# Kernel tuning notes

Hardware: AMD Instinct MI355X
Metric: run time of the kernel (lower is better)

## Reference

```python
import jax, jax.numpy as jnp
import numpy as np

N_NODES = 50000
N_EDGES = 1600000
N_GRAPHS = 64
IN_DIM = 128
HID = 128
N_CLASSES = 10


def setup_inputs() -> dict:
    key = jax.random.key(0)
    ks = jax.random.split(key, 12)
    x = jax.random.normal(ks[0], (N_NODES, IN_DIM), dtype=jnp.float32)
    edge_index = jax.random.randint(ks[1], (2, N_EDGES), 0, N_NODES, dtype=jnp.int32)
    batch = jnp.sort(jax.random.randint(ks[2], (N_NODES,), 0, N_GRAPHS, dtype=jnp.int32))
    def glorot(k, shape):
        s = 1.0 / np.sqrt(shape[0])
        return jax.random.uniform(k, shape, jnp.float32, -s, s)
    W1 = glorot(ks[3], (IN_DIM, HID)); b1 = jnp.zeros((HID,), jnp.float32)
    W2 = glorot(ks[4], (HID, HID));    b2 = jnp.zeros((HID,), jnp.float32)
    Wc1 = glorot(ks[5], (HID, HID));   bc1 = glorot(ks[6], (HID,))
    Wc2 = glorot(ks[7], (HID, N_CLASSES)); bc2 = glorot(ks[8], (N_CLASSES,))
    return {"x": x, "edge_index": edge_index, "batch": batch,
            "W1": W1, "b1": b1, "W2": W2, "b2": b2,
            "Wc1": Wc1, "bc1": bc1, "Wc2": Wc2, "bc2": bc2}


def gcn_conv(x, edge_index, W, b):
    """PyG GCNConv: sym-normalized A-hat (with self loops) @ (x W) + b."""
    n = x.shape[0]
    loop = jnp.arange(n, dtype=edge_index.dtype)
    src = jnp.concatenate([edge_index[0], loop])  # message source
    dst = jnp.concatenate([edge_index[1], loop])  # message target
    deg = jax.ops.segment_sum(jnp.ones_like(src, dtype=x.dtype), dst, num_segments=n)
    dinv = jnp.where(deg > 0, jax.lax.rsqrt(deg), jnp.zeros_like(deg))
    norm = dinv[src] * dinv[dst]  # [E+N]
    h = x @ W                     # [N, H]
    msg = h[src] * norm[:, None]  # gather + scale
    out = jax.ops.segment_sum(msg, dst, num_segments=n)
    return out + b


def reference(x, edge_index, batch, W1, b1, W2, b2, Wc1, bc1, Wc2, bc2):
    h = jax.nn.relu(gcn_conv(x, edge_index, W1, b1))
    h = jax.nn.relu(gcn_conv(h, edge_index, W2, b2))
    # per-graph mean pooling (segment mean)
    sums = jax.ops.segment_sum(h, batch, num_segments=N_GRAPHS)
    cnt = jax.ops.segment_sum(jnp.ones((h.shape[0],), h.dtype), batch, num_segments=N_GRAPHS)
    g = sums / jnp.clip(cnt, 1.0)[:, None]  # [G, H]
    z = jax.nn.relu(g @ Wc1 + bc1)
    return z @ Wc2 + bc2
```

## Files before the change

kernel.cpp:

```cpp
#include <hip/hip_runtime.h>
#include <cstdint>
#include <cstddef>

#define CHUNK 8192

typedef __attribute__((ext_vector_type(8))) short short8;
typedef __attribute__((ext_vector_type(4))) float f32x4;
typedef __attribute__((ext_vector_type(2))) float f32x2;
typedef __attribute__((ext_vector_type(4))) unsigned int u32x4;

__device__ __forceinline__ float bf2f(unsigned short u) {
  return __uint_as_float(((unsigned)u) << 16);
}
__device__ __forceinline__ unsigned short f2bf(float f) {
  unsigned u = __float_as_uint(f);
  u += 0x7fffu + ((u >> 16) & 1u);
  return (unsigned short)(u >> 16);
}
__device__ __forceinline__ f32x2 unpk(unsigned u) {
  f32x2 r;
  r.x = __uint_as_float(u << 16);
  r.y = __uint_as_float(u & 0xffff0000u);
  return r;
}
__device__ __forceinline__ void pkfma(f32x2& a, f32x2 b, f32x2 c) {
  asm("v_pk_fma_f32 %0, %1, %2, %0" : "+v"(a) : "v"(b), "v"(c));
}

union SMem {
  unsigned short ws[128 * 136];
  struct { int c[256]; int cur[256]; int sb[256];
           unsigned short colL[12288]; } cf;
};

__global__ void prep_k(const float* __restrict__ W1, const float* __restrict__ W2,
                       unsigned short* __restrict__ W1t, unsigned short* __restrict__ W2t,
                       int* __restrict__ gcur, int B,
                       float* __restrict__ gsums, int GN) {
  int idx = blockIdx.x * 256 + threadIdx.x;
  const float* W = (idx < 16384) ? W1 : W2;
  unsigned short* Wt = (idx < 16384) ? W1t : W2t;
  int i = idx & 16383;
  int k = i >> 7, n = i & 127;
  Wt[n * 128 + k] = f2bf(W[i]);
  if (blockIdx.x == 0 && threadIdx.x < B) gcur[threadIdx.x] = 0;
  if (idx < GN) gsums[idx] = 0.f;
}

__global__ __launch_bounds__(512) void scatter_sort_k(const int* __restrict__ src,
                                                      const int* __restrict__ dst, int E,
                                                      int* __restrict__ gcur,
                                                      unsigned int* __restrict__ tmp,
                                                      int cap, int B) {
  __shared__ unsigned sorted[CHUNK];
  __shared__ int h[256];
  __shared__ int lps[256];
  __shared__ int base_s[256];
  __shared__ int cur[256];
  int t = threadIdx.x;
  if (t < 256) h[t] = 0;
  __syncthreads();
  int e0 = blockIdx.x * CHUNK;
  int e1 = e0 + CHUNK; if (e1 > E) e1 = E;
  int m = e1 - e0;
  for (int i = t; i < m; i += 512) {
    atomicAdd(&h[dst[e0 + i] >> 8], 1);
  }
  __syncthreads();
  int v = (t < 256) ? h[t] : 0;
  if (t < 256) lps[t] = v;
  __syncthreads();
  for (int off = 1; off < 256; off <<= 1) {
    int u = (t >= off && t < 256) ? lps[t - off] : 0;
    __syncthreads();
    if (t < 256) lps[t] += u;
    __syncthreads();
  }
  int incl = (t < 256) ? lps[t] : 0;
  if (t < B && v > 0) base_s[t] = atomicAdd(&gcur[t], v);
  if (t < 256) {
    cur[t] = 0;
    lps[t] = incl - v;
  }
  __syncthreads();
  for (int i = t; i < m; i += 512) {
    int d = dst[e0 + i], s = src[e0 + i];
    int b = d >> 8;
    int r = atomicAdd(&cur[b], 1);
    sorted[lps[b] + r] = ((unsigned)b << 24) | ((unsigned)s << 8) | (unsigned)(d & 255);
  }
  __syncthreads();
  for (int i = t; i < m; i += 512) {
    unsigned u = sorted[i];
    int b = u >> 24;
    int p = base_s[b] + (i - lps[b]);
    if (p < cap) tmp[(size_t)b * cap + p] = u;
  }
}

template <bool AF32>
__device__ __forceinline__ void gemm_tile(SMem& sm, const void* Ap,
                                          const unsigned short* Wt,
                                          unsigned short* C, int N, int tile) {
  for (int idx = threadIdx.x; idx < 2048; idx += 512) {
    int n = idx >> 4, c = idx & 15;
    *(uint4*)&sm.ws[n * 136 + c * 8] = ((const uint4*)Wt)[idx];
  }
  __syncthreads();
  const int w = threadIdx.x >> 6;
  const int lane = threadIdx.x & 63;
  const int quad = lane >> 4, l16 = lane & 15;
  const int r = tile * 128 + w * 16 + l16;
  f32x4 acc[8] = {};
  #pragma unroll
  for (int ks = 0; ks < 4; ks++) {
    short8 a = {};
    if (r < N) {
      if (AF32) {
        const float* ar = (const float*)Ap + (size_t)r * 128 + ks * 32 + quad * 8;
        float4 u0 = *(const float4*)ar;
        float4 u1 = *(const float4*)(ar + 4);
        a[0] = (short)f2bf(u0.x); a[1] = (short)f2bf(u0.y);
        a[2] = (short)f2bf(u0.z); a[3] = (short)f2bf(u0.w);
        a[4] = (short)f2bf(u1.x); a[5] = (short)f2bf(u1.y);
        a[6] = (short)f2bf(u1.z); a[7] = (short)f2bf(u1.w);
      } else {
        a = *(const short8*)((const unsigned short*)Ap + (size_t)r * 128 + ks * 32 + quad * 8);
      }
    }
    #pragma unroll
    for (int t = 0; t < 8; t++) {
      short8 bF = *(const short8*)&sm.ws[(t * 16 + l16) * 136 + ks * 32 + quad * 8];
      acc[t] = __builtin_amdgcn_mfma_f32_16x16x32_bf16(a, bF, acc[t], 0, 0, 0);
    }
  }
  __syncthreads();
  unsigned short* Cs = sm.ws;
  {
    int rloc = w * 16 + quad * 4;
    #pragma unroll
    for (int t = 0; t < 8; t++)
      #pragma unroll
      for (int rg = 0; rg < 4; rg++)
        Cs[(rloc + rg) * 132 + t * 16 + l16] = f2bf(acc[t][rg]);
  }
  __syncthreads();
  const int r0 = tile * 128;
  for (int idx = threadIdx.x; idx < 2048; idx += 512) {
    int row = idx >> 4, c = idx & 15;
    int rr = r0 + row;
    if (rr < N) {
      uint2 a = *(uint2*)&Cs[row * 132 + c * 8];
      uint2 b = *(uint2*)&Cs[row * 132 + c * 8 + 4];
      ((uint4*)C)[(size_t)rr * 16 + c] = make_uint4(a.x, a.y, b.x, b.y);
    }
  }
}

__global__ __launch_bounds__(512) void cntfill_gemm1_k(const unsigned int* __restrict__ tmp,
                                                       const int* __restrict__ gcur,
                                                       int N, int E, int cap, int B,
                                                       float* __restrict__ dinv,
                                                       int* __restrict__ rs,
                                                       unsigned short* __restrict__ col,
                                                       const float* __restrict__ x,
                                                       const unsigned short* __restrict__ W1t,
                                                       unsigned short* __restrict__ B2) {
  __shared__ SMem sm;
  const int t = threadIdx.x;
  if ((int)blockIdx.x >= B) {
    gemm_tile<true>(sm, x, W1t, B2, N, blockIdx.x - B);
    return;
  }
  int b = blockIdx.x;
  int cb = 0;
  if (t < B) { cb = gcur[t]; if (cb > cap) cb = cap; }
  if (t < 256) sm.cf.sb[t] = cb;
  __syncthreads();
  for (int off = 1; off < 256; off <<= 1) {
    int u = (t >= off && t < 256) ? sm.cf.sb[t - off] : 0;
    __syncthreads();
    if (t < 256) sm.cf.sb[t] += u;
    __syncthreads();
  }
  int base_b = (b > 0) ? sm.cf.sb[b - 1] : 0;
  int cnt_b = sm.cf.sb[b] - base_b;
  if (b == 0 && t == 0) rs[N] = sm.cf.sb[B - 1];
  const unsigned* tb = tmp + (size_t)b * cap;
  if (t < 256) sm.cf.c[t] = 0;
  __syncthreads();
  for (int i = t; i < cnt_b; i += 512) atomicAdd(&sm.cf.c[tb[i] & 255u], 1);
  __syncthreads();
  int v = (t < 256) ? sm.cf.c[t] : 0;
  if (t < 256) sm.cf.cur[t] = v;
  __syncthreads();
  for (int off = 1; off < 256; off <<= 1) {
    int u = (t >= off && t < 256) ? sm.cf.cur[t - off] : 0;
    __syncthreads();
    if (t < 256) sm.cf.cur[t] += u;
    __syncthreads();
  }
  int rsv = (t < 256) ? (base_b + sm.cf.cur[t] - v) : 0;
  int node = (b << 8) + t;
  if (t < 256 && node < N) {
    rs[node] = rsv;
    dinv[node] = rsqrtf((float)v + 1.0f);
  }
  __syncthreads();
  if (cnt_b <= 12288) {
    if (t < 256) sm.cf.cur[t] = rsv - base_b;
    __syncthreads();
    for (int i = t; i < cnt_b; i += 512) {
      unsigned u = tb[i];
      int lpos = atomicAdd(&sm.cf.cur[u & 255u], 1);
      sm.cf.colL[lpos] = (unsigned short)((u >> 8) & 0xFFFFu);
    }
    __syncthreads();
    for (int i = t; i < cnt_b; i += 512) col[base_b + i] = sm.cf.colL[i];
  } else {
    if (t < 256) sm.cf.cur[t] = rsv;
    __syncthreads();
    for (int i = t; i < cnt_b; i += 512) {
      unsigned u = tb[i];
      int pos = atomicAdd(&sm.cf.cur[u & 255u], 1);
      col[pos] = (unsigned short)((u >> 8) & 0xFFFFu);
    }
  }
}

template <bool AF32>
__global__ __launch_bounds__(512) void gemm_bf_k(const void* __restrict__ Ap,
                                                 const unsigned short* __restrict__ Wt,
                                                 unsigned short* __restrict__ C, int N) {
  __shared__ SMem sm;
  gemm_tile<AF32>(sm, Ap, Wt, C, N, blockIdx.x);
}

template <typename CT>
__device__ __forceinline__ void agg_body(f32x2 (&acc2)[4],
                                         const unsigned short* __restrict__ h,
                                         const CT* __restrict__ col,
                                         const float* __restrict__ dinv,
                                         int beg, int end, int g, int l) {
  int base = beg;
  for (; base + 32 <= end; base += 32) {
    int s[8];
    float w[8];
    uint4 H[8];
    #pragma unroll
    for (int k = 0; k < 8; k++) s[k] = (int)col[base + 4 * k + g];
    #pragma unroll
    for (int k = 0; k < 8; k++) w[k] = dinv[s[k]];
    #pragma unroll
    for (int k = 0; k < 8; k++) H[k] = ((const uint4*)(h + (size_t)s[k] * 128))[l];
    #pragma unroll
    for (int k = 0; k < 8; k++) {
      f32x2 wv; wv.x = w[k]; wv.y = w[k];
      pkfma(acc2[0], unpk(H[k].x), wv);
      pkfma(acc2[1], unpk(H[k].y), wv);
      pkfma(acc2[2], unpk(H[k].z), wv);
      pkfma(acc2[3], unpk(H[k].w), wv);
    }
  }
  for (; base < end; base += 16) {
    int e0 = base + g, e1 = base + 4 + g, e2 = base + 8 + g, e3 = base + 12 + g;
    int i0 = (e0 < end) ? e0 : end - 1;
    int i1 = (e1 < end) ? e1 : end - 1;
    int i2 = (e2 < end) ? e2 : end - 1;
    int i3 = (e3 < end) ? e3 : end - 1;
    int s0 = (int)col[i0], s1 = (int)col[i1], s2 = (int)col[i2], s3 = (int)col[i3];
    float w0 = (e0 < end) ? dinv[s0] : 0.f;
    float w1 = (e1 < end) ? dinv[s1] : 0.f;
    float w2 = (e2 < end) ? dinv[s2] : 0.f;
    float w3 = (e3 < end) ? dinv[s3] : 0.f;
    uint4 h0 = ((const uint4*)(h + (size_t)s0 * 128))[l];
    uint4 h1 = ((const uint4*)(h + (size_t)s1 * 128))[l];
    uint4 h2 = ((const uint4*)(h + (size_t)s2 * 128))[l];
    uint4 h3 = ((const uint4*)(h + (size_t)s3 * 128))[l];
    f32x2 w0v; w0v.x = w0; w0v.y = w0;
    f32x2 w1v; w1v.x = w1; w1v.y = w1;
    f32x2 w2v; w2v.x = w2; w2v.y = w2;
    f32x2 w3v; w3v.x = w3; w3v.y = w3;
    pkfma(acc2[0], unpk(h0.x), w0v); pkfma(acc2[0], unpk(h1.x), w1v);
    pkfma(acc2[0], unpk(h2.x), w2v); pkfma(acc2[0], unpk(h3.x), w3v);
    pkfma(acc2[1], unpk(h0.y), w0v); pkfma(acc2[1], unpk(h1.y), w1v);
    pkfma(acc2[1], unpk(h2.y), w2v); pkfma(acc2[1], unpk(h3.y), w3v);
    pkfma(acc2[2], unpk(h0.z), w0v); pkfma(acc2[2], unpk(h1.z), w1v);
    pkfma(acc2[2], unpk(h2.z), w2v); pkfma(acc2[2], unpk(h3.z), w3v);
    pkfma(acc2[3], unpk(h0.w), w0v); pkfma(acc2[3], unpk(h1.w), w1v);
    pkfma(acc2[3], unpk(h2.w), w2v); pkfma(acc2[3], unpk(h3.w), w3v);
  }
  #pragma unroll
  for (int j = 0; j < 4; j++) {
    acc2[j].x += __shfl_xor(acc2[j].x, 16);
    acc2[j].y += __shfl_xor(acc2[j].y, 16);
    acc2[j].x += __shfl_xor(acc2[j].x, 32);
    acc2[j].y += __shfl_xor(acc2[j].y, 32);
  }
}

template <typename CT>
__global__ __launch_bounds__(256) void agg32_k(const unsigned short* __restrict__ h,
                                               const int* __restrict__ rs,
                                               const CT* __restrict__ col,
                                               const float* __restrict__ dinv,
                                               const float* __restrict__ bias,
                                               unsigned short* __restrict__ outp, int n) {
  int wid = (blockIdx.x * blockDim.x + threadIdx.x) >> 6;
  int lane = threadIdx.x & 63;
  if (wid >= n) return;
  const int g = lane >> 4;
  const int l = lane & 15;
  float di = dinv[wid];
  f32x2 acc2[4];
  {
    uint4 sv = ((const uint4*)(h + (size_t)wid * 128))[l];
    float ws = (g == 0) ? di : 0.f;
    f32x2 wv; wv.x = ws; wv.y = ws;
    acc2[0] = unpk(sv.x) * wv;
    acc2[1] = unpk(sv.y) * wv;
    acc2[2] = unpk(sv.z) * wv;
    acc2[3] = unpk(sv.w) * wv;
  }
  agg_body<CT>(acc2, h, col, dinv, rs[wid], rs[wid + 1], g, l);
  if (g == 0) {
    float4 bA = *(const float4*)(bias + l * 8);
    float4 bB = *(const float4*)(bias + l * 8 + 4);
    float r0 = fmaxf(acc2[0].x * di + bA.x, 0.f);
    float r1 = fmaxf(acc2[0].y * di + bA.y, 0.f);
    float r2 = fmaxf(acc2[1].x * di + bA.z, 0.f);
    float r3 = fmaxf(acc2[1].y * di + bA.w, 0.f);
    float r4 = fmaxf(acc2[2].x * di + bB.x, 0.f);
    float r5 = fmaxf(acc2[2].y * di + bB.y, 0.f);
    float r6 = fmaxf(acc2[3].x * di + bB.z, 0.f);
    float r7 = fmaxf(acc2[3].y * di + bB.w, 0.f);
    u32x4 v;
    v.x = (unsigned)f2bf(r0) | ((unsigned)f2bf(r1) << 16);
    v.y = (unsigned)f2bf(r2) | ((unsigned)f2bf(r3) << 16);
    v.z = (unsigned)f2bf(r4) | ((unsigned)f2bf(r5) << 16);
    v.w = (unsigned)f2bf(r6) | ((unsigned)f2bf(r7) << 16);
    __builtin_nontemporal_store(v, (u32x4*)outp + (size_t)wid * 16 + l);
  }
}

#define SPLITS 8
__global__ __launch_bounds__(256) void pool_sum_k(const unsigned short* __restrict__ h,
                                                  const int* __restrict__ bat, int n,
                                                  float* __restrict__ gsums) {
  __shared__ float red[16][136];
  const int g = blockIdx.x / SPLITS;
  const int sp = blockIdx.x % SPLITS;
  const int t = threadIdx.x;
  const int slot = t >> 4;
  const int seg = t & 15;
  int lo;
  {
    int l = 0, r = n;
    while (l < r) { int m = (l + r) >> 1; if (bat[m] < g) l = m + 1; else r = m; }
    lo = l;
  }
  int hi;
  {
    int l = lo, r = n;
    while (l < r) { int m = (l + r) >> 1; if (bat[m] < g + 1) l = m + 1; else r = m; }
    hi = l;
  }
  int L = hi - lo;
  int chunk = (L + SPLITS - 1) / SPLITS;
  int i0 = lo + sp * chunk;
  int i1 = i0 + chunk; if (i1 > hi) i1 = hi;
  if (i0 >= i1) return;
  float a0 = 0.f, a1 = 0.f, a2 = 0.f, a3 = 0.f, a4 = 0.f, a5 = 0.f, a6 = 0.f, a7 = 0.f;
  for (int i = i0 + slot; i < i1; i += 16) {
    uint4 v = ((const uint4*)(h + (size_t)i * 128))[seg];
    a0 += bf2f((unsigned short)v.x);  a1 += bf2f((unsigned short)(v.x >> 16));
    a2 += bf2f((unsigned short)v.y);  a3 += bf2f((unsigned short)(v.y >> 16));
    a4 += bf2f((unsigned short)v.z);  a5 += bf2f((unsigned short)(v.z >> 16));
    a6 += bf2f((unsigned short)v.w);  a7 += bf2f((unsigned short)(v.w >> 16));
  }
  red[slot][seg * 8 + 0] = a0; red[slot][seg * 8 + 1] = a1;
  red[slot][seg * 8 + 2] = a2; red[slot][seg * 8 + 3] = a3;
  red[slot][seg * 8 + 4] = a4; red[slot][seg * 8 + 5] = a5;
  red[slot][seg * 8 + 6] = a6; red[slot][seg * 8 + 7] = a7;
  __syncthreads();
  if (t < 128) {
    float s = 0.f;
    #pragma unroll
    for (int k = 0; k < 16; k++) s += red[k][t];
    unsafeAtomicAdd(&gsums[g * 128 + t], s);
  }
}

__global__ __launch_bounds__(256) void classify_k(const float* __restrict__ gsums,
                                                  const int* __restrict__ bat, int n,
                                                  const float* __restrict__ Wc1,
                                                  const float* __restrict__ bc1,
                                                  const float* __restrict__ Wc2,
                                                  const float* __restrict__ bc2,
                                                  float* __restrict__ out, int nc) {
  __shared__ float gs[128];
  __shared__ float zs[128];
  const int g = blockIdx.x;
  const int t = threadIdx.x;
  int lo;
  {
    int l = 0, r = n;
    while (l < r) { int m = (l + r) >> 1; if (bat[m] < g) l = m + 1; else r = m; }
    lo = l;
  }
  int hi;
  {
    int l = lo, r = n;
    while (l < r) { int m = (l + r) >> 1; if (bat[m] < g + 1) l = m + 1; else r = m; }
    hi = l;
  }
  if (t < 128) {
    float c = (float)(hi - lo); if (c < 1.f) c = 1.f;
    gs[t] = gsums[g * 128 + t] / c;
  }
  __syncthreads();
  if (t < 128) {
    float a = bc1[t];
    for (int k = 0; k < 128; k++) a += gs[k] * Wc1[k * 128 + t];
    zs[t] = fmaxf(a, 0.f);
  }
  __syncthreads();
  if (t < nc) {
    float o = bc2[t];
    for (int k = 0; k < 128; k++) o += zs[k] * Wc2[k * nc + t];
    out[g * nc + t] = o;
  }
}

__global__ __launch_bounds__(256) void poolclassify2_k(const unsigned short* __restrict__ h,
                                                       const int* __restrict__ bat, int n,
                                                       const float* __restrict__ Wc1,
                                                       const float* __restrict__ bc1,
                                                       const float* __restrict__ Wc2,
                                                       const float* __restrict__ bc2,
                                                       float* __restrict__ out, int nc) {
  __shared__ float red[16][136];
  __shared__ float gs[128];
  __shared__ float zs[128];
  const int g = blockIdx.x;
  const int t = threadIdx.x;
  const int slot = t >> 4;
  const int seg = t & 15;
  int lo;
  {
    int l = 0, r = n;
    while (l < r) { int m = (l + r) >> 1; if (bat[m] < g) l = m + 1; else r = m; }
    lo = l;
  }
  int hi;
  {
    int l = lo, r = n;
    while (l < r) { int m = (l + r) >> 1; if (bat[m] < g + 1) l = m + 1; else r = m; }
    hi = l;
  }
  float a0 = 0.f, a1 = 0.f, a2 = 0.f, a3 = 0.f, a4 = 0.f, a5 = 0.f, a6 = 0.f, a7 = 0.f;
  for (int i = lo + slot; i < hi; i += 16) {
    uint4 v = ((const uint4*)(h + (size_t)i * 128))[seg];
    a0 += bf2f((unsigned short)v.x);  a1 += bf2f((unsigned short)(v.x >> 16));
    a2 += bf2f((unsigned short)v.y);  a3 += bf2f((unsigned short)(v.y >> 16));
    a4 += bf2f((unsigned short)v.z);  a5 += bf2f((unsigned short)(v.z >> 16));
    a6 += bf2f((unsigned short)v.w);  a7 += bf2f((unsigned short)(v.w >> 16));
  }
  red[slot][seg * 8 + 0] = a0; red[slot][seg * 8 + 1] = a1;
  red[slot][seg * 8 + 2] = a2; red[slot][seg * 8 + 3] = a3;
  red[slot][seg * 8 + 4] = a4; red[slot][seg * 8 + 5] = a5;
  red[slot][seg * 8 + 6] = a6; red[slot][seg * 8 + 7] = a7;
  __syncthreads();
  if (t < 128) {
    float c = (float)(hi - lo); if (c < 1.f) c = 1.f;
    float s = 0.f;
    #pragma unroll
    for (int k = 0; k < 16; k++) s += red[k][t];
    gs[t] = s / c;
  }
  __syncthreads();
  if (t < 128) {
    float a = bc1[t];
    for (int k = 0; k < 128; k++) a += gs[k] * Wc1[k * 128 + t];
    zs[t] = fmaxf(a, 0.f);
  }
  __syncthreads();
  if (t < nc) {
    float o = bc2[t];
    for (int k = 0; k < 128; k++) o += zs[k] * Wc2[k * nc + t];
    out[g * nc + t] = o;
  }
}

__global__ void count_edges_k(const int* __restrict__ dst, int E, int* __restrict__ cnt) {
  int e = blockIdx.x * blockDim.x + threadIdx.x;
  if (e < E) atomicAdd(&cnt[dst[e]], 1);
}
__global__ void dinv_k(const int* __restrict__ cnt, float* __restrict__ dinv, int n) {
  int i = blockIdx.x * blockDim.x + threadIdx.x;
  if (i < n) dinv[i] = rsqrtf((float)cnt[i] + 1.0f);
}
__global__ void fill_csr_k(const int* __restrict__ src, const int* __restrict__ dst, int E,
                           int* __restrict__ cursor, int* __restrict__ col) {
  int e = blockIdx.x * blockDim.x + threadIdx.x;
  if (e < E) {
    int d = dst[e], s = src[e];
    int pos = atomicAdd(&cursor[d], 1);
    col[pos] = s;
  }
}
__global__ void scan1_k(const int* __restrict__ cnt, int* __restrict__ rs,
                        int* __restrict__ partials, int n) {
  __shared__ int s[1024];
  int t = threadIdx.x;
  int gid = blockIdx.x * 1024 + t;
  int v = (gid < n) ? cnt[gid] : 0;
  s[t] = v;
  __syncthreads();
  for (int off = 1; off < 1024; off <<= 1) {
    int u = (t >= off) ? s[t - off] : 0;
    __syncthreads();
    s[t] += u;
    __syncthreads();
  }
  if (gid < n) rs[gid] = s[t] - v;
  if (t == 1023) partials[blockIdx.x] = s[1023];
}
__global__ void scan2_k(int* __restrict__ partials, int nb) {
  if (threadIdx.x == 0 && blockIdx.x == 0) {
    int acc = 0;
    for (int i = 0; i < nb; i++) { int v = partials[i]; partials[i] = acc; acc += v; }
  }
}
__global__ void scan3_k(int* __restrict__ rs, int* __restrict__ cursor,
                        const int* __restrict__ partials, int n, int total) {
  int gid = blockIdx.x * blockDim.x + threadIdx.x;
  if (gid < n) {
    int v = rs[gid] + partials[gid >> 10];
    rs[gid] = v;
    cursor[gid] = v;
  }
  if (gid == 0) rs[n] = total;
}

extern "C" void kernel_launch(void* const* d_in, const int* in_sizes, int n_in,
                              void* d_out, int out_size, void* d_ws, size_t ws_size,
                              hipStream_t stream) {
  const float* x   = (const float*)d_in[0];
  const int*   ei  = (const int*)d_in[1];
  const int*   bat = (const int*)d_in[2];
  const float* W1  = (const float*)d_in[3];
  const float* b1  = (const float*)d_in[4];
  const float* W2  = (const float*)d_in[5];
  const float* b2  = (const float*)d_in[6];
  const float* Wc1 = (const float*)d_in[7];
  const float* bc1 = (const float*)d_in[8];
  const float* Wc2 = (const float*)d_in[9];
  const float* bc2 = (const float*)d_in[10];
  float* out = (float*)d_out;

  const int N  = in_sizes[0] / 128;
  const int E  = in_sizes[1] / 2;
  const int NC = in_sizes[10];
  const int G  = out_size / NC;
  const int* src = ei;
  const int* dst = ei + E;
  (void)n_in; (void)ws_size;

  size_t off = 0;
  auto walloc = [&](size_t bytes) -> void* {
    void* p = (char*)d_ws + off;
    off += (bytes + 255) & ~(size_t)255;
    return p;
  };
  unsigned short* B2 = (unsigned short*)walloc((size_t)N * 128 * 2);
  unsigned short* B3 = (unsigned short*)walloc((size_t)N * 128 * 2);
  unsigned short* W1t = (unsigned short*)walloc(128 * 128 * 2);
  unsigned short* W2t = (unsigned short*)walloc(128 * 128 * 2);
  float* dinv = (float*)walloc((size_t)N * 4);
  int*   rs   = (int*)  walloc((size_t)(N + 1) * 4);
  float* gsums = (float*)walloc((size_t)G * 128 * 4);

  const bool small = (N <= 65535);
  const int gblocks = (N + 127) / 128;
  const int aggGrid = (N + 3) / 4;

  if (small) {
    const int B    = (N + 255) >> 8;
    const int nblk = (E + CHUNK - 1) / CHUNK;
    const int cap  = (E + B - 1) / B + 2048;
    unsigned short* col = (unsigned short*)walloc((size_t)E * 2);
    unsigned int*   tmp = (unsigned int*)  walloc((size_t)B * cap * 4);
    int* gcur = (int*)walloc((size_t)B * 4);

    prep_k<<<128, 256, 0, stream>>>(W1, W2, W1t, W2t, gcur, B, gsums, G * 128);
    scatter_sort_k<<<nblk, 512, 0, stream>>>(src, dst, E, gcur, tmp, cap, B);
    cntfill_gemm1_k<<<B + gblocks, 512, 0, stream>>>(tmp, gcur, N, E, cap, B,
                                                     dinv, rs, col, x, W1t, B2);
    agg32_k<unsigned short><<<aggGrid, 256, 0, stream>>>(B2, rs, col, dinv, b1, B3, N);
    gemm_bf_k<false><<<gblocks, 512, 0, stream>>>(B3, W2t, B2, N);
    agg32_k<unsigned short><<<aggGrid, 256, 0, stream>>>(B2, rs, col, dinv, b2, B3, N);
    pool_sum_k<<<G * SPLITS, 256, 0, stream>>>(B3, bat, N, gsums);
    classify_k<<<G, 256, 0, stream>>>(gsums, bat, N, Wc1, bc1, Wc2, bc2, out, NC);
  } else {
    const int nb = (N + 1023) / 1024;
    int* cnt    = (int*)walloc((size_t)N * 4);
    int* cursor = (int*)walloc((size_t)N * 4);
    int* col    = (int*)walloc((size_t)E * 4);
    int* partials = (int*)walloc(256 * 4);
    prep_k<<<128, 256, 0, stream>>>(W1, W2, W1t, W2t, cnt , 0, gsums, G * 128);
    (void)hipMemsetAsync(cnt, 0, (size_t)N * 4, stream);
    count_edges_k<<<(E + 255) / 256, 256, 0, stream>>>(dst, E, cnt);
    scan1_k<<<nb, 1024, 0, stream>>>(cnt, rs, partials, N);
    scan2_k<<<1, 64, 0, stream>>>(partials, nb);
    scan3_k<<<(N + 255) / 256, 256, 0, stream>>>(rs, cursor, partials, N, E);
    dinv_k<<<(N + 255) / 256, 256, 0, stream>>>(cnt, dinv, N);
    fill_csr_k<<<(E + 255) / 256, 256, 0, stream>>>(src, dst, E, cursor, col);

    gemm_bf_k<true><<<gblocks, 512, 0, stream>>>(x, W1t, B2, N);
    agg32_k<int><<<aggGrid, 256, 0, stream>>>(B2, rs, col, dinv, b1, B3, N);
    gemm_bf_k<false><<<gblocks, 512, 0, stream>>>(B3, W2t, B2, N);
    agg32_k<int><<<aggGrid, 256, 0, stream>>>(B2, rs, col, dinv, b2, B3, N);
    poolclassify2_k<<<G, 256, 0, stream>>>(B3, bat, N, Wc1, bc1, Wc2, bc2, out, NC);
  }
}
```

Measured before the change: 263.3 us.

## Remove prep kernel and split first GEMM across scatter and count kernels

Drops the separate weight-prep launch. Gcur and gsums are now zeroed with one memset, and the first GEMM reads fp32 W1 directly, transposing and converting it to bf16 in shared memory. Part of the first GEMM's tiles (3/5) and the W2 transpose now run as extra blocks inside the edge scatter-sort kernel. The remaining GEMM tiles run alongside the count/fill kernel. The aim is to save a launch and overlap dense GEMM work with the bandwidth- and atomic-bound sort phases. The cost is that each GEMM block converts W1 from scalar fp32 loads itself, and the larger shared-memory union may reduce occupancy.

```diff
diff --git a/kernel.cpp b/kernel.cpp
--- a/kernel.cpp
+++ b/kernel.cpp
@@ -27,8 +27,10 @@
   asm("v_pk_fma_f32 %0, %1, %2, %0" : "+v"(a) : "v"(b), "v"(c));
 }
 
-union SMem {
+union SMemX {
   unsigned short ws[128 * 136];
+  struct { unsigned sorted[CHUNK];
+           int h[256]; int lps[256]; int base_s[256]; int cur[256]; } sc;
   struct { int c[256]; int cur[256]; int sb[256];
            unsigned short colL[12288]; } cf;
 };
@@ -47,64 +49,22 @@
   if (idx < GN) gsums[idx] = 0.f;
 }
 
-__global__ __launch_bounds__(512) void scatter_sort_k(const int* __restrict__ src,
-                                                      const int* __restrict__ dst, int E,
-                                                      int* __restrict__ gcur,
-                                                      unsigned int* __restrict__ tmp,
-                                                      int cap, int B) {
-  __shared__ unsigned sorted[CHUNK];
-  __shared__ int h[256];
-  __shared__ int lps[256];
-  __shared__ int base_s[256];
-  __shared__ int cur[256];
-  int t = threadIdx.x;
-  if (t < 256) h[t] = 0;
-  __syncthreads();
-  int e0 = blockIdx.x * CHUNK;
-  int e1 = e0 + CHUNK; if (e1 > E) e1 = E;
-  int m = e1 - e0;
-  for (int i = t; i < m; i += 512) {
-    atomicAdd(&h[dst[e0 + i] >> 8], 1);
-  }
-  __syncthreads();
-  int v = (t < 256) ? h[t] : 0;
-  if (t < 256) lps[t] = v;
-  __syncthreads();
-  for (int off = 1; off < 256; off <<= 1) {
-    int u = (t >= off && t < 256) ? lps[t - off] : 0;
-    __syncthreads();
-    if (t < 256) lps[t] += u;
-    __syncthreads();
-  }
-  int incl = (t < 256) ? lps[t] : 0;
-  if (t < B && v > 0) base_s[t] = atomicAdd(&gcur[t], v);
-  if (t < 256) {
-    cur[t] = 0;
-    lps[t] = incl - v;
-  }
-  __syncthreads();
-  for (int i = t; i < m; i += 512) {
-    int d = dst[e0 + i], s = src[e0 + i];
-    int b = d >> 8;
-    int r = atomicAdd(&cur[b], 1);
-    sorted[lps[b] + r] = ((unsigned)b << 24) | ((unsigned)s << 8) | (unsigned)(d & 255);
-  }
-  __syncthreads();
-  for (int i = t; i < m; i += 512) {
-    unsigned u = sorted[i];
-    int b = u >> 24;
-    int p = base_s[b] + (i - lps[b]);
-    if (p < cap) tmp[(size_t)b * cap + p] = u;
-  }
-}
-
-template <bool AF32>
-__device__ __forceinline__ void gemm_tile(SMem& sm, const void* Ap,
-                                          const unsigned short* Wt,
+template <bool AF32, bool WF32>
+__device__ __forceinline__ void gemm_tile(SMemX& sm, const void* Ap,
+                                          const void* Wp,
                                           unsigned short* C, int N, int tile) {
-  for (int idx = threadIdx.x; idx < 2048; idx += 512) {
-    int n = idx >> 4, c = idx & 15;
-    *(uint4*)&sm.ws[n * 136 + c * 8] = ((const uint4*)Wt)[idx];
+  if (WF32) {
+    const float* Wf = (const float*)Wp;
+    for (int idx = threadIdx.x; idx < 16384; idx += 512) {
+      int k = idx >> 7, n = idx & 127;
+      sm.ws[n * 136 + k] = f2bf(Wf[idx]);
+    }
+  } else {
+    const unsigned short* Wt = (const unsigned short*)Wp;
+    for (int idx = threadIdx.x; idx < 2048; idx += 512) {
+      int n = idx >> 4, c = idx & 15;
+      *(uint4*)&sm.ws[n * 136 + c * 8] = ((const uint4*)Wt)[idx];
+    }
   }
   __syncthreads();
   const int w = threadIdx.x >> 6;
@@ -157,19 +117,88 @@
   }
 }
 
-__global__ __launch_bounds__(512) void cntfill_gemm1_k(const unsigned int* __restrict__ tmp,
-                                                       const int* __restrict__ gcur,
-                                                       int N, int E, int cap, int B,
-                                                       float* __restrict__ dinv,
-                                                       int* __restrict__ rs,
-                                                       unsigned short* __restrict__ col,
-                                                       const float* __restrict__ x,
-                                                       const unsigned short* __restrict__ W1t,
-                                                       unsigned short* __restrict__ B2) {
-  __shared__ SMem sm;
+__global__ __launch_bounds__(512) void scat_gemm1a_k(const int* __restrict__ src,
+                                                     const int* __restrict__ dst, int E,
+                                                     int* __restrict__ gcur,
+                                                     unsigned int* __restrict__ tmp,
+                                                     int cap, int B,
+                                                     const float* __restrict__ x,
+                                                     const float* __restrict__ W1,
+                                                     unsigned short* __restrict__ B2, int N,
+                                                     int nblk, int T1,
+                                                     const float* __restrict__ W2,
+                                                     unsigned short* __restrict__ W2t,
+                                                     int P2) {
+  __shared__ SMemX sm;
+  const int t = threadIdx.x;
+  const int bid = blockIdx.x;
+  if (bid >= nblk) {
+    int gb = bid - nblk;
+    if (gb < T1) {
+      gemm_tile<true, true>(sm, x, W1, B2, N, gb);
+    } else {
+      int base = (gb - T1) * 512 + t;
+      for (int i = base; i < 16384; i += P2 * 512) {
+        int k = i >> 7, n = i & 127;
+        W2t[n * 128 + k] = f2bf(W2[i]);
+      }
+    }
+    return;
+  }
+  if (t < 256) sm.sc.h[t] = 0;
+  __syncthreads();
+  int e0 = bid * CHUNK;
+  int e1 = e0 + CHUNK; if (e1 > E) e1 = E;
+  int m = e1 - e0;
+  for (int i = t; i < m; i += 512) {
+    atomicAdd(&sm.sc.h[dst[e0 + i] >> 8], 1);
+  }
+  __syncthreads();
+  int v = (t < 256) ? sm.sc.h[t] : 0;
+  if (t < 256) sm.sc.lps[t] = v;
+  __syncthreads();
+  for (int off = 1; off < 256; off <<= 1) {
+    int u = (t >= off && t < 256) ? sm.sc.lps[t - off] : 0;
+    __syncthreads();
+    if (t < 256) sm.sc.lps[t] += u;
+    __syncthreads();
+  }
+  int incl = (t < 256) ? sm.sc.lps[t] : 0;
+  if (t < B && v > 0) sm.sc.base_s[t] = atomicAdd(&gcur[t], v);
+  if (t < 256) {
+    sm.sc.cur[t] = 0;
+    sm.sc.lps[t] = incl - v;
+  }
+  __syncthreads();
+  for (int i = t; i < m; i += 512) {
+    int d = dst[e0 + i], s = src[e0 + i];
+    int b = d >> 8;
+    int r = atomicAdd(&sm.sc.cur[b], 1);
+    sm.sc.sorted[sm.sc.lps[b] + r] = ((unsigned)b << 24) | ((unsigned)s << 8) | (unsigned)(d & 255);
+  }
+  __syncthreads();
+  for (int i = t; i < m; i += 512) {
+    unsigned u = sm.sc.sorted[i];
+    int b = u >> 24;
+    int p = sm.sc.base_s[b] + (i - sm.sc.lps[b]);
+    if (p < cap) tmp[(size_t)b * cap + p] = u;
+  }
+}
+
+__global__ __launch_bounds__(512) void cnt_gemm1b_k(const unsigned int* __restrict__ tmp,
+                                                    const int* __restrict__ gcur,
+                                                    int N, int E, int cap, int B,
+                                                    float* __restrict__ dinv,
+                                                    int* __restrict__ rs,
+                                                    unsigned short* __restrict__ col,
+                                                    const float* __restrict__ x,
+                                                    const float* __restrict__ W1,
+                                                    unsigned short* __restrict__ B2,
+                                                    int T1) {
+  __shared__ SMemX sm;
   const int t = threadIdx.x;
   if ((int)blockIdx.x >= B) {
-    gemm_tile<true>(sm, x, W1t, B2, N, blockIdx.x - B);
+    gemm_tile<true, true>(sm, x, W1, B2, N, T1 + (int)blockIdx.x - B);
     return;
   }
   int b = blockIdx.x;
@@ -228,12 +257,12 @@
   }
 }
 
-template <bool AF32>
+template <bool AF32, bool WF32>
 __global__ __launch_bounds__(512) void gemm_bf_k(const void* __restrict__ Ap,
-                                                 const unsigned short* __restrict__ Wt,
+                                                 const void* __restrict__ Wp,
                                                  unsigned short* __restrict__ C, int N) {
-  __shared__ SMem sm;
-  gemm_tile<AF32>(sm, Ap, Wt, C, N, blockIdx.x);
+  __shared__ SMemX sm;
+  gemm_tile<AF32, WF32>(sm, Ap, Wp, C, N, blockIdx.x);
 }
 
 template <typename CT>
@@ -580,6 +609,7 @@
   float* dinv = (float*)walloc((size_t)N * 4);
   int*   rs   = (int*)  walloc((size_t)(N + 1) * 4);
   float* gsums = (float*)walloc((size_t)G * 128 * 4);
+  int*   gcur  = (int*)walloc(256 * 4);
 
   const bool small = (N <= 65535);
   const int gblocks = (N + 127) / 128;
@@ -589,16 +619,18 @@
     const int B    = (N + 255) >> 8;
     const int nblk = (E + CHUNK - 1) / CHUNK;
     const int cap  = (E + B - 1) / B + 2048;
+    const int T1   = (gblocks * 3) / 5;
+    const int P2   = 8;
     unsigned short* col = (unsigned short*)walloc((size_t)E * 2);
     unsigned int*   tmp = (unsigned int*)  walloc((size_t)B * cap * 4);
-    int* gcur = (int*)walloc((size_t)B * 4);
-
-    prep_k<<<128, 256, 0, stream>>>(W1, W2, W1t, W2t, gcur, B, gsums, G * 128);
-    scatter_sort_k<<<nblk, 512, 0, stream>>>(src, dst, E, gcur, tmp, cap, B);
-    cntfill_gemm1_k<<<B + gblocks, 512, 0, stream>>>(tmp, gcur, N, E, cap, B,
-                                                     dinv, rs, col, x, W1t, B2);
+
+    (void)hipMemsetAsync(gsums, 0, (size_t)G * 128 * 4 + 1024, stream);
+    scat_gemm1a_k<<<nblk + T1 + P2, 512, 0, stream>>>(src, dst, E, gcur, tmp, cap, B,
+                                                      x, W1, B2, N, nblk, T1, W2, W2t, P2);
+    cnt_gemm1b_k<<<B + (gblocks - T1), 512, 0, stream>>>(tmp, gcur, N, E, cap, B,
+                                                         dinv, rs, col, x, W1, B2, T1);
     agg32_k<unsigned short><<<aggGrid, 256, 0, stream>>>(B2, rs, col, dinv, b1, B3, N);
-    gemm_bf_k<false><<<gblocks, 512, 0, stream>>>(B3, W2t, B2, N);
+    gemm_bf_k<false, false><<<gblocks, 512, 0, stream>>>(B3, W2t, B2, N);
     agg32_k<unsigned short><<<aggGrid, 256, 0, stream>>>(B2, rs, col, dinv, b2, B3, N);
     pool_sum_k<<<G * SPLITS, 256, 0, stream>>>(B3, bat, N, gsums);
     classify_k<<<G, 256, 0, stream>>>(gsums, bat, N, Wc1, bc1, Wc2, bc2, out, NC);
@@ -617,9 +649,9 @@
     dinv_k<<<(N + 255) / 256, 256, 0, stream>>>(cnt, dinv, N);
     fill_csr_k<<<(E + 255) / 256, 256, 0, stream>>>(src, dst, E, cursor, col);
 
-    gemm_bf_k<true><<<gblocks, 512, 0, stream>>>(x, W1t, B2, N);
+    gemm_bf_k<true, false><<<gblocks, 512, 0, stream>>>(x, W1t, B2, N);
     agg32_k<int><<<aggGrid, 256, 0, stream>>>(B2, rs, col, dinv, b1, B3, N);
-    gemm_bf_k<false><<<gblocks, 512, 0, stream>>>(B3, W2t, B2, N);
+    gemm_bf_k<false, false><<<gblocks, 512, 0, stream>>>(B3, W2t, B2, N);
     agg32_k<int><<<aggGrid, 256, 0, stream>>>(B2, rs, col, dinv, b2, B3, N);
     poolclassify2_k<<<G, 256, 0, stream>>>(B3, bat, N, Wc1, bc1, Wc2, bc2, out, NC);
   }
```

Result: no change. 259.2 us, median of 2 (-1.5%).
